# Optimization experiments

Measured on AMD Instinct MI355X. Metric: run time of the kernel, lower is better.

Reference implementation:

```python
import jax, jax.numpy as jnp
import numpy as np

EMBED = 1024
HEADS = 16
HEAD_DIM = EMBED // HEADS
MAX_SEQ = 5000
THETA = 10000.0
BATCH = 16
SEQ_K = 1024
SEQ_Q = 512


def _rope_tables():
    inv = 1.0 / (THETA ** (np.arange(0, EMBED, 2)[: EMBED // 2] / EMBED))
    ang = np.outer(np.arange(MAX_SEQ), inv)  # [MAX_SEQ, EMBED//2]
    return jnp.asarray(np.cos(ang), jnp.float32), jnp.asarray(np.sin(ang), jnp.float32)

COS_T, SIN_T = _rope_tables()


def _apply_rope(x, idx):
    # x: [B, S, E]; idx: [B, S]; pairs are (x[...,2i], x[...,2i+1]) across the FULL embed dim
    B, S, E = x.shape
    xp = x.reshape(B, S, E // 2, 2)
    xr, xi = xp[..., 0], xp[..., 1]
    c, s = COS_T[idx], SIN_T[idx]  # [B, S, E//2]
    return jnp.stack([xr * c - xi * s, xr * s + xi * c], axis=-1).reshape(B, S, E)


def _attn_mask(key_padding_mask):
    # (causal triu OR key padding) AND NOT eye  (eye keeps diagonal attendable), then cut query rows
    tri = jnp.triu(jnp.ones((SEQ_K, SEQ_K), bool), k=1)
    m = jnp.logical_or(tri[None], key_padding_mask[:, None, :])  # [B, K, K]
    m = jnp.logical_and(m, ~jnp.eye(SEQ_K, dtype=bool)[None])
    return m[:, -SEQ_Q:, :]  # [B, Q, K]


def setup_inputs() -> dict:
    key = jax.random.key(0)
    ks = jax.random.split(key, 16)
    def lin(i):
        W = jax.random.normal(ks[i], (EMBED, EMBED), jnp.float32) / np.sqrt(EMBED).astype(np.float32)
        b = jnp.zeros((EMBED,), jnp.float32)
        return W, b
    Wq, bq = lin(0); Wk, bk = lin(1); Wv, bv = lin(2); Wo, bo = lin(3)
    Wxr, bxr = lin(4); Wyr, byr = lin(5)
    Wxz, bxz = lin(6); Wyz, byz = lin(7)
    Wxg, bxg = lin(8); Wyg, byg = lin(9)
    key_in = jax.random.normal(ks[10], (BATCH, SEQ_K, EMBED), jnp.float32)
    key_index = jnp.sort(jax.random.randint(ks[11], (BATCH, SEQ_K), 0, MAX_SEQ), axis=-1)
    key_padding_mask = jax.random.randint(ks[12], (BATCH, SEQ_K), 0, 2).astype(bool)
    return dict(key_in=key_in, key_index=key_index, key_padding_mask=key_padding_mask,
                Wq=Wq, bq=bq, Wk=Wk, bk=bk, Wv=Wv, bv=bv, Wo=Wo, bo=bo,
                Wxr=Wxr, bxr=bxr, Wyr=Wyr, byr=byr, Wxz=Wxz, bxz=bxz,
                Wyz=Wyz, byz=byz, Wxg=Wxg, bxg=bxg, Wyg=Wyg, byg=byg)


def reference(key_in, key_index, key_padding_mask,
              Wq, bq, Wk, bk, Wv, bv, Wo, bo,
              Wxr, bxr, Wyr, byr, Wxz, bxz, Wyz, byz, Wxg, bxg, Wyg, byg):
    B = key_in.shape[0]
    # cut_query=True: query is the last SEQ_Q steps of key
    query = key_in[:, -SEQ_Q:]
    q_idx = key_index[:, -SEQ_Q:]
    q = query @ Wq + bq
    k = key_in @ Wk + bk
    v = key_in @ Wv + bv
    # RoPE applied on full embed dim BEFORE head split (as in source)
    q = _apply_rope(q, q_idx)
    k = _apply_rope(k, key_index)
    qh = q.reshape(B, SEQ_Q, HEADS, HEAD_DIM)
    kh = k.reshape(B, SEQ_K, HEADS, HEAD_DIM)
    vh = v.reshape(B, SEQ_K, HEADS, HEAD_DIM)
    mask = _attn_mask(key_padding_mask)  # [B, Q, K]
    bias = jnp.where(mask, -jnp.inf, 0.0).astype(key_in.dtype)[:, None]  # [B,1,Q,K]
    scores = jnp.einsum('bqhd,bkhd->bhqk', qh, kh) / np.float32(np.sqrt(HEAD_DIM)) + bias
    w = jax.nn.softmax(scores, axis=-1)  # [B,H,Q,K]
    o = jnp.einsum('bhqk,bkhd->bqhd', w, vh).reshape(B, SEQ_Q, EMBED)
    o = o @ Wo + bo
    # GRU-style gated residual combine (use_residual=True, use_gated=True)
    x = query
    r = jax.nn.sigmoid(x @ Wxr + bxr + o @ Wyr + byr)
    z = jax.nn.sigmoid(x @ Wxz + bxz + o @ Wyz + byz)
    h = jnp.tanh((r * x) @ Wxg + bxg + o @ Wyg + byg)
    out = (1.0 - z) * x + z * h
    attn_weights = w.mean(axis=1)  # averaged over heads, [B, Q, K]
    return out, attn_weights
```

## Files before the change

### kernel.cpp

```cpp
#include <hip/hip_runtime.h>
#include <hip/hip_bf16.h>


typedef __attribute__((ext_vector_type(8))) short bf16x8;
typedef __attribute__((ext_vector_type(4))) float f32x4;

__device__ __forceinline__ short f2bs(float f) {
  union { __hip_bfloat16 h; short s; } u; u.h = __float2bfloat16(f); return u.s;
}

static constexpr size_t OFF_WT   = 0;
static constexpr size_t OFF_TAB  = 20971520;
static constexpr size_t OFF_XBF  = 41451520;
static constexpr size_t OFF_QH   = 75005952;
static constexpr size_t OFF_KH   = 91783168;
static constexpr size_t OFF_VT   = 125337600;
static constexpr size_t OFF_OAT  = 158892032;
static constexpr size_t OFF_O2   = 175669248;
static constexpr size_t OFF_INV  = OFF_OAT;
static constexpr size_t OFF_RBZB = 75005952;
static constexpr size_t OFF_RX   = 142114816;
static constexpr size_t OFF_HB   = OFF_XBF;

__device__ __forceinline__ int swz(int q) { return ((q & 3) << 3) ^ ((q & 12) << 2); }

__global__ __launch_bounds__(256) void k_cvtx(const float* __restrict__ x,
                                              short* __restrict__ xbf) {
  size_t i = ((size_t)blockIdx.x * 256 + threadIdx.x) * 8;
  f32x4 a = *(const f32x4*)(x + i);
  f32x4 b = *(const f32x4*)(x + i + 4);
  bf16x8 o;
  o[0] = f2bs(a[0]); o[1] = f2bs(a[1]); o[2] = f2bs(a[2]); o[3] = f2bs(a[3]);
  o[4] = f2bs(b[0]); o[5] = f2bs(b[1]); o[6] = f2bs(b[2]); o[7] = f2bs(b[3]);
  *(bf16x8*)(xbf + i) = o;
}

__global__ void k_tabinv(double* __restrict__ inv) {
  int i = threadIdx.x;
  inv[i] = pow(10000.0, -(double)i / 512.0);
}
__global__ __launch_bounds__(256) void k_table(float* __restrict__ tab,
                                               const double* __restrict__ inv) {
  int i = blockIdx.x * 256 + threadIdx.x;
  if (i >= 5000 * 512) return;
  int pos = i >> 9, fi = i & 511;
  double ds, dc;
  sincos((double)pos * inv[fi], &ds, &dc);
  tab[2 * i] = (float)dc;
  tab[2 * i + 1] = (float)ds;
}

struct W10 { const float* p[10]; };
__global__ __launch_bounds__(256) void k_wt(W10 wsrc, short* __restrict__ wt) {
  __shared__ short t[32][33];
  int kb = blockIdx.x * 32, nb = blockIdx.y * 32, wi = blockIdx.z;
  const float* src = wsrc.p[wi];
  int tid = threadIdx.x;
#pragma unroll
  for (int e = 0; e < 4; ++e) {
    int idx = e * 256 + tid;
    int kr = idx >> 5, nc = idx & 31;
    t[nc][kr] = f2bs(src[(size_t)(kb + kr) * 1024 + nb + nc]);
  }
  __syncthreads();
  short* dst = wt + (size_t)wi * 1024 * 1024;
#pragma unroll
  for (int e = 0; e < 4; ++e) {
    int idx = e * 256 + tid;
    int nr = idx >> 5, kc = idx & 31;
    dst[(size_t)(nb + nr) * 1024 + kb + kc] = t[nr][kc];
  }
}

enum { CM_BF16 = 0, CM_F32 = 2, CM_F32ACC = 3, CM_VT = 4, CM_ROPE = 5 };

template <int AMODE, int CMODE>
__global__ __launch_bounds__(256) void k_gemm(
    const short* __restrict__ A, const short* __restrict__ Bt,
    const float* __restrict__ bias, const float* __restrict__ bias2,
    void* __restrict__ Cout, int ldc,
    const float* __restrict__ tab, const int* __restrict__ kidx,
    int sshift, int qoff) {
  __shared__ __align__(16) short lA[128 * 32];
  __shared__ __align__(16) short lB[128 * 32];
  const int tid = threadIdx.x;
  const int lane = tid & 63;
  const int wv = tid >> 6;
  const int wm = wv >> 1, wn = wv & 1;
  const int lo = lane & 15, hi = lane >> 4;
  const int tm0 = blockIdx.x * 128;
  const int tn0 = blockIdx.y * 128;

  const f32x4 vz = {0.f, 0.f, 0.f, 0.f};
  f32x4 acc[4][4];
#pragma unroll
  for (int m = 0; m < 4; ++m)
#pragma unroll
    for (int n = 0; n < 4; ++n) acc[m][n] = vz;

  for (int kt = 0; kt < 32; ++kt) {
    const int k0 = kt * 32;
    __syncthreads();
#pragma unroll
    for (int i = 0; i < 2; ++i) {
      int f = i * 256 + tid;
      int r = f >> 2;
      int cb = (f & 3) * 16;
      int arow = tm0 + r;
      if (AMODE) arow = ((arow >> 9) << 10) + 512 + (arow & 511);
      const char* ga = (const char*)(A + (size_t)arow * 1024 + k0) + cb;
      __builtin_amdgcn_global_load_lds(
          (const __attribute__((address_space(1))) void*)ga,
          (__attribute__((address_space(3))) void*)((char*)lA + (size_t)(i * 256 + wv * 64) * 16),
          16, 0, 0);
      int brow = tn0 + r;
      const char* gb = (const char*)(Bt + (size_t)brow * 1024 + k0) + cb;
      __builtin_amdgcn_global_load_lds(
          (const __attribute__((address_space(1))) void*)gb,
          (__attribute__((address_space(3))) void*)((char*)lB + (size_t)(i * 256 + wv * 64) * 16),
          16, 0, 0);
    }
    __syncthreads();
    bf16x8 af[4], bfr[4];
#pragma unroll
    for (int m = 0; m < 4; ++m)
      af[m] = *(const bf16x8*)&lA[(wm * 64 + m * 16 + lo) * 32 + hi * 8];
#pragma unroll
    for (int n = 0; n < 4; ++n)
      bfr[n] = *(const bf16x8*)&lB[(wn * 64 + n * 16 + lo) * 32 + hi * 8];
#pragma unroll
    for (int m = 0; m < 4; ++m)
#pragma unroll
      for (int n = 0; n < 4; ++n)
        acc[m][n] = __builtin_amdgcn_mfma_f32_16x16x32_bf16(af[m], bfr[n], acc[m][n], 0, 0, 0);
  }

  if constexpr (CMODE == CM_ROPE) {
    __hip_bfloat16* out = (__hip_bfloat16*)Cout;
    const float2* t2 = (const float2*)tab;
    const int srows = 1 << sshift;
    const float sgn = (lane & 1) ? 1.f : -1.f;
#pragma unroll
    for (int m = 0; m < 4; ++m) {
      int row_base = tm0 + wm * 64 + m * 16 + hi * 4;
#pragma unroll
      for (int n = 0; n < 4; ++n) {
        int col = tn0 + wn * 64 + n * 16 + lo;
        float bsv = bias[col];
        int j = col >> 1, hh = col >> 6, dd = col & 63;
#pragma unroll
        for (int r = 0; r < 4; ++r) {
          int row = row_base + r;
          int bb = row >> sshift, ss = row & (srows - 1);
          int idx = kidx[bb * 1024 + qoff + ss];
          float2 cs = t2[(size_t)idx * 512 + j];
          float val = acc[m][n][r] + bsv;
          float part = __shfl_xor(val, 1);
          float rot = val * cs.x + sgn * part * cs.y;
          out[((size_t)(bb * 16 + hh) * srows + ss) * 64 + dd] = __float2bfloat16(rot);
        }
      }
    }
  } else if constexpr (CMODE == CM_VT) {
    __hip_bfloat16* out = (__hip_bfloat16*)Cout;
#pragma unroll
    for (int m = 0; m < 4; ++m) {
      int row_base = tm0 + wm * 64 + m * 16 + hi * 4;
#pragma unroll
      for (int n = 0; n < 4; ++n) {
        int col = tn0 + wn * 64 + n * 16 + lo;
        float bsv = bias[col];
        int hh = col >> 6, dd = col & 63;
#pragma unroll
        for (int r = 0; r < 4; ++r) {
          int row = row_base + r;
          int bb = row >> 10, ss = row & 1023;
          out[((size_t)(bb * 16 + hh) * 64 + dd) * 1024 + ss] =
              __float2bfloat16(acc[m][n][r] + bsv);
        }
      }
    }
  } else if constexpr (CMODE == CM_F32 || CMODE == CM_F32ACC) {
    float* out = (float*)Cout;
#pragma unroll
    for (int m = 0; m < 4; ++m) {
      int row_base = tm0 + wm * 64 + m * 16 + hi * 4;
#pragma unroll
      for (int n = 0; n < 4; ++n) {
        int col = tn0 + wn * 64 + n * 16 + lo;
        float bsv = (col < 1024 || !bias2) ? bias[col] : bias2[col - 1024];
#pragma unroll
        for (int r = 0; r < 4; ++r) {
          size_t off = (size_t)(row_base + r) * ldc + col;
          float val = acc[m][n][r] + bsv;
          if constexpr (CMODE == CM_F32ACC) val += out[off];
          out[off] = val;
        }
      }
    }
  } else {
    __hip_bfloat16* out = (__hip_bfloat16*)Cout;
#pragma unroll
    for (int m = 0; m < 4; ++m) {
      int row_base = tm0 + wm * 64 + m * 16 + hi * 4;
#pragma unroll
      for (int n = 0; n < 4; ++n) {
        int col = tn0 + wn * 64 + n * 16 + lo;
        float bsv = bias[col];
#pragma unroll
        for (int r = 0; r < 4; ++r) {
          size_t off = (size_t)(row_base + r) * ldc + col;
          out[off] = __float2bfloat16(acc[m][n][r] + bsv);
        }
      }
    }
  }
}

__global__ __launch_bounds__(512, 2) void k_attn(
    const __hip_bfloat16* __restrict__ qh,
    const __hip_bfloat16* __restrict__ kh,
    const __hip_bfloat16* __restrict__ vt,
    const unsigned char* __restrict__ padraw,
    float* __restrict__ mean_out,
    __hip_bfloat16* __restrict__ oat) {
  __shared__ float Sld[16 * 1024];
  __shared__ float osc[4 * 64 * 4];
  short* Pld = (short*)Sld;
  const int wgid = blockIdx.x;
  const int b = wgid & 15, qt = wgid >> 4;
  const int tid = threadIdx.x, lane = tid & 63, wv = tid >> 6;
  const int lo = lane & 15, hi = lane >> 4;
  const int wg = wv & 3, half = wv >> 2;
  const f32x4 vz = {0.f, 0.f, 0.f, 0.f};

  bool is_byte = false;
#pragma unroll
  for (int j = 1; j < 256; ++j)
    if ((j & 3) && padraw[j] == 1) is_byte = true;
  const int* ipad = (const int*)padraw;

  unsigned pmask = 0;
#pragma unroll
  for (int nt = 0; nt < 8; ++nt) {
    int kpos = wv * 128 + nt * 16 + lo;
    int pk = is_byte ? (int)padraw[b * 1024 + kpos]
                     : (ipad[b * 1024 + kpos] != 0 ? 1 : 0);
    pmask |= (unsigned)(pk != 0) << nt;
  }

  float macc[2][16];
#pragma unroll
  for (int rr = 0; rr < 2; ++rr)
#pragma unroll
    for (int i = 0; i < 16; ++i) macc[rr][i] = 0.f;

  const __hip_bfloat16* qbase =
      qh + ((size_t)(b * 16) * 512 + (size_t)qt * 16) * 64;
  bf16x8 qf0 = *(const bf16x8*)(qbase + (size_t)lo * 64 + hi * 8);
  bf16x8 qf1 = *(const bf16x8*)(qbase + (size_t)lo * 64 + 32 + hi * 8);

  for (int h = 0; h < 16; ++h) {
    const __hip_bfloat16* kbh = kh + (size_t)(b * 16 + h) * 1024 * 64;
    const __hip_bfloat16* vbh = vt + (size_t)(b * 16 + h) * 64 * 1024;

    bf16x8 kbuf[2][2];
#pragma unroll
    for (int p = 0; p < 2; ++p) {
      int kr = wv * 128 + p * 16 + lo;
      kbuf[p][0] = *(const bf16x8*)(kbh + (size_t)kr * 64 + hi * 8);
      kbuf[p][1] = *(const bf16x8*)(kbh + (size_t)kr * 64 + 32 + hi * 8);
    }
#pragma unroll
    for (int nt = 0; nt < 8; ++nt) {
      bf16x8 ck0 = kbuf[nt & 1][0], ck1 = kbuf[nt & 1][1];
      if (nt < 6) {
        int kr = wv * 128 + (nt + 2) * 16 + lo;
        kbuf[nt & 1][0] = *(const bf16x8*)(kbh + (size_t)kr * 64 + hi * 8);
        kbuf[nt & 1][1] = *(const bf16x8*)(kbh + (size_t)kr * 64 + 32 + hi * 8);
      }
      f32x4 sa = vz;
      sa = __builtin_amdgcn_mfma_f32_16x16x32_bf16(qf0, ck0, sa, 0, 0, 0);
      sa = __builtin_amdgcn_mfma_f32_16x16x32_bf16(qf1, ck1, sa, 0, 0, 0);
      int kpos = wv * 128 + nt * 16 + lo;
      int pk = (pmask >> nt) & 1;
#pragma unroll
      for (int r = 0; r < 4; ++r) {
        int q = hi * 4 + r;
        int qg = 512 + qt * 16 + q;
        float sv = sa[r] * 0.125f;
        bool msk = (kpos > qg) || (kpos < qg && pk != 0);
        Sld[q * 1024 + (kpos ^ swz(q))] = msk ? -1e30f : sv;
      }
    }
    __syncthreads();

#pragma unroll
    for (int rr = 0; rr < 2; ++rr) {
      int q = wv * 2 + rr;
      const int c = swz(q);
      float* row = Sld + q * 1024;
      float v[16], mx = -1e30f;
#pragma unroll
      for (int i = 0; i < 16; ++i) {
        v[i] = row[(lane + i * 64) ^ c];
        mx = fmaxf(mx, v[i]);
      }
#pragma unroll
      for (int off = 32; off > 0; off >>= 1) mx = fmaxf(mx, __shfl_xor(mx, off));
      float sum = 0.f;
#pragma unroll
      for (int i = 0; i < 16; ++i) { v[i] = __expf(v[i] - mx); sum += v[i]; }
#pragma unroll
      for (int off = 32; off > 0; off >>= 1) sum += __shfl_xor(sum, off);
      float invs = 1.0f / sum;
      short* prow = Pld + q * 2048 + 1024;
#pragma unroll
      for (int i = 0; i < 16; ++i) {
        float p = v[i] * invs;
        prow[(lane + i * 64) ^ c] = f2bs(p);
        macc[rr][i] += p;
      }
    }
    __syncthreads();

    f32x4 oacc = vz;
    {
      const short* prow = Pld + lo * 2048 + 1024;
      const int cl = swz(lo);
      const int kcg = half * 16;
      const __hip_bfloat16* vrow = vbh + (size_t)(wg * 16 + lo) * 1024;
      bf16x8 vbuf[2];
#pragma unroll
      for (int p = 0; p < 2; ++p)
        vbuf[p] = *(const bf16x8*)(vrow + (kcg + p) * 32 + hi * 8);
#pragma unroll
      for (int kc = 0; kc < 16; ++kc) {
        bf16x8 cv = vbuf[kc & 1];
        if (kc < 14)
          vbuf[kc & 1] = *(const bf16x8*)(vrow + (kcg + kc + 2) * 32 + hi * 8);
        bf16x8 pa = *(const bf16x8*)&prow[((kcg + kc) * 32 + hi * 8) ^ cl];
        oacc = __builtin_amdgcn_mfma_f32_16x16x32_bf16(pa, cv, oacc, 0, 0, 0);
      }
    }

    if (h < 15) {
      const __hip_bfloat16* qn = qbase + (size_t)(h + 1) * 512 * 64;
      qf0 = *(const bf16x8*)(qn + (size_t)lo * 64 + hi * 8);
      qf1 = *(const bf16x8*)(qn + (size_t)lo * 64 + 32 + hi * 8);
    }

    if (half == 1) {
#pragma unroll
      for (int r = 0; r < 4; ++r) osc[(wg * 64 + lane) * 4 + r] = oacc[r];
    }
    __syncthreads();
    if (half == 0) {
#pragma unroll
      for (int r = 0; r < 4; ++r) {
        float o = oacc[r] + osc[(wg * 64 + lane) * 4 + r];
        int q = qt * 16 + hi * 4 + r;
        oat[((size_t)b * 512 + q) * 1024 + h * 64 + wg * 16 + lo] =
            __float2bfloat16(o);
      }
    }
  }

#pragma unroll
  for (int rr = 0; rr < 2; ++rr) {
    size_t mrow = ((size_t)b * 512 + (size_t)qt * 16 + wv * 2 + rr) * 1024;
#pragma unroll
    for (int i = 0; i < 16; ++i)
      mean_out[mrow + lane + i * 64] = macc[rr][i] * 0.0625f;
  }
}

__global__ __launch_bounds__(256) void k_rx(const float* __restrict__ RbZb,
                                            const float* __restrict__ x,
                                            short* __restrict__ rx) {
  size_t base = ((size_t)blockIdx.x * 256 + threadIdx.x) * 4;
  int row = (int)(base >> 10), col = (int)(base & 1023);
  int b = row >> 9, s = row & 511;
  const float* xp = x + ((size_t)(b * 1024 + 512 + s) << 10) + col;
  f32x4 rv = *(const f32x4*)(RbZb + (size_t)row * 2048 + col);
  f32x4 xv = *(const f32x4*)xp;
  typedef __attribute__((ext_vector_type(4))) short s16x4;
  s16x4 o;
#pragma unroll
  for (int j = 0; j < 4; ++j) {
    float r = 1.f / (1.f + __expf(-rv[j]));
    o[j] = f2bs(r * xv[j]);
  }
  *(s16x4*)(rx + base) = o;
}

__global__ __launch_bounds__(256) void k_final(const float* __restrict__ RbZb,
                                               const float* __restrict__ Hb,
                                               const float* __restrict__ x,
                                               float* __restrict__ out0) {
  size_t base = ((size_t)blockIdx.x * 256 + threadIdx.x) * 4;
  int row = (int)(base >> 10), col = (int)(base & 1023);
  int b = row >> 9, s = row & 511;
  const float* xp = x + ((size_t)(b * 1024 + 512 + s) << 10) + col;
  f32x4 zv = *(const f32x4*)(RbZb + (size_t)row * 2048 + 1024 + col);
  f32x4 hv = *(const f32x4*)(Hb + base);
  f32x4 xv = *(const f32x4*)xp;
  f32x4 o;
#pragma unroll
  for (int j = 0; j < 4; ++j) {
    float z = 1.f / (1.f + __expf(-zv[j]));
    float hh = tanhf(hv[j]);
    o[j] = (1.f - z) * xv[j] + z * hh;
  }
  *(f32x4*)(out0 + base) = o;
}

extern "C" void kernel_launch(void* const* d_in, const int* in_sizes, int n_in,
                              void* d_out, int out_size, void* d_ws, size_t ws_size,
                              hipStream_t stream) {
  const float* key_in = (const float*)d_in[0];
  const int* key_index = (const int*)d_in[1];
  const unsigned char* pad = (const unsigned char*)d_in[2];
  const float* bq  = (const float*)d_in[4];
  const float* bk  = (const float*)d_in[6];
  const float* bv  = (const float*)d_in[8];
  const float* bo  = (const float*)d_in[10];
  const float* bxr = (const float*)d_in[12];
  const float* byr = (const float*)d_in[14];
  const float* bxz = (const float*)d_in[16];
  const float* byz = (const float*)d_in[18];
  const float* bxg = (const float*)d_in[20];
  const float* byg = (const float*)d_in[22];

  char* ws = (char*)d_ws;
  short* wt = (short*)(ws + OFF_WT);
  float* tab = (float*)(ws + OFF_TAB);
  short* xbf = (short*)(ws + OFF_XBF);
  __hip_bfloat16* qh = (__hip_bfloat16*)(ws + OFF_QH);
  __hip_bfloat16* kh = (__hip_bfloat16*)(ws + OFF_KH);
  __hip_bfloat16* vt = (__hip_bfloat16*)(ws + OFF_VT);
  double* inv = (double*)(ws + OFF_INV);
  float* RbZb = (float*)(ws + OFF_RBZB);
  __hip_bfloat16* oat = (__hip_bfloat16*)(ws + OFF_OAT);
  short* o2 = (short*)(ws + OFF_O2);
  short* rx = (short*)(ws + OFF_RX);
  float* Hb = (float*)(ws + OFF_HB);

  float* out0 = (float*)d_out;
  float* out1 = out0 + (size_t)8388608;

  W10 wargs;
  wargs.p[0] = (const float*)d_in[3];
  wargs.p[1] = (const float*)d_in[5];
  wargs.p[2] = (const float*)d_in[7];
  wargs.p[3] = (const float*)d_in[9];
  wargs.p[4] = (const float*)d_in[11];
  wargs.p[5] = (const float*)d_in[15];
  wargs.p[6] = (const float*)d_in[13];
  wargs.p[7] = (const float*)d_in[17];
  wargs.p[8] = (const float*)d_in[19];
  wargs.p[9] = (const float*)d_in[21];

  k_cvtx<<<8192, 256, 0, stream>>>(key_in, xbf);
  k_wt<<<dim3(32, 32, 10), 256, 0, stream>>>(wargs, wt);
  k_tabinv<<<1, 512, 0, stream>>>(inv);
  k_table<<<10000, 256, 0, stream>>>(tab, inv);

  k_gemm<1, CM_ROPE><<<dim3(64, 8), 256, 0, stream>>>(
      xbf, wt + (size_t)0 * 1048576, bq, nullptr, (void*)qh, 0, tab, key_index, 9, 512);
  k_gemm<0, CM_ROPE><<<dim3(128, 8), 256, 0, stream>>>(
      xbf, wt + (size_t)1 * 1048576, bk, nullptr, (void*)kh, 0, tab, key_index, 10, 0);
  k_gemm<0, CM_VT><<<dim3(128, 8), 256, 0, stream>>>(
      xbf, wt + (size_t)2 * 1048576, bv, nullptr, (void*)vt, 0, nullptr, nullptr, 0, 0);

  k_attn<<<dim3(512), 512, 0, stream>>>(qh, kh, vt, pad, out1, oat);

  k_gemm<0, CM_BF16><<<dim3(64, 8), 256, 0, stream>>>(
      (const short*)oat, wt + (size_t)3 * 1048576, bo, nullptr, (void*)o2, 1024,
      nullptr, nullptr, 0, 0);
  k_gemm<1, CM_F32><<<dim3(64, 16), 256, 0, stream>>>(
      xbf, wt + (size_t)4 * 1048576, bxr, bxz, (void*)RbZb, 2048,
      nullptr, nullptr, 0, 0);
  k_gemm<0, CM_F32ACC><<<dim3(64, 16), 256, 0, stream>>>(
      o2, wt + (size_t)6 * 1048576, byr, byz, (void*)RbZb, 2048,
      nullptr, nullptr, 0, 0);
  k_rx<<<8192, 256, 0, stream>>>(RbZb, key_in, rx);
  k_gemm<0, CM_F32><<<dim3(64, 8), 256, 0, stream>>>(
      rx, wt + (size_t)8 * 1048576, bxg, nullptr, (void*)Hb, 1024,
      nullptr, nullptr, 0, 0);
  k_gemm<0, CM_F32ACC><<<dim3(64, 8), 256, 0, stream>>>(
      o2, wt + (size_t)9 * 1048576, byg, nullptr, (void*)Hb, 1024,
      nullptr, nullptr, 0, 0);
  k_final<<<8192, 256, 0, stream>>>(RbZb, Hb, key_in, out0);
}
```

Baseline: 768.4 us.

## Skip fully masked causal key tiles in attention QK, softmax and PV

After: 2.313 ms. 3.01x slower.

```diff
diff --git a/kernel.cpp b/kernel.cpp
--- a/kernel.cpp
+++ b/kernel.cpp
@@ -234,6 +234,11 @@
   const int wg = wv & 3, half = wv >> 2;
   const f32x4 vz = {0.f, 0.f, 0.f, 0.f};
 
+  const int gmax = 32 + qt;
+  const int nchunks = (gmax + 4) >> 2;
+  const int gpad = nchunks * 4 - 1;
+  const int ntv = ((gmax - wv) >> 3) + 1;
+
   bool is_byte = false;
 #pragma unroll
   for (int j = 1; j < 256; ++j)
@@ -243,7 +248,7 @@
   unsigned pmask = 0;
 #pragma unroll
   for (int nt = 0; nt < 8; ++nt) {
-    int kpos = wv * 128 + nt * 16 + lo;
+    int kpos = (nt * 8 + wv) * 16 + lo;
     int pk = is_byte ? (int)padraw[b * 1024 + kpos]
                      : (ipad[b * 1024 + kpos] != 0 ? 1 : 0);
     pmask |= (unsigned)(pk != 0) << nt;
@@ -264,25 +269,37 @@
     const __hip_bfloat16* kbh = kh + (size_t)(b * 16 + h) * 1024 * 64;
     const __hip_bfloat16* vbh = vt + (size_t)(b * 16 + h) * 64 * 1024;
 
+    for (int g = gmax + 1; g <= gpad; ++g) {
+      if ((g & 7) == wv) {
+        int kpos = g * 16 + lo;
+#pragma unroll
+        for (int r = 0; r < 4; ++r) {
+          int q = hi * 4 + r;
+          Sld[q * 1024 + (kpos ^ swz(q))] = -1e30f;
+        }
+      }
+    }
+
     bf16x8 kbuf[2][2];
 #pragma unroll
     for (int p = 0; p < 2; ++p) {
-      int kr = wv * 128 + p * 16 + lo;
+      int kr = (p * 8 + wv) * 16 + lo;
       kbuf[p][0] = *(const bf16x8*)(kbh + (size_t)kr * 64 + hi * 8);
       kbuf[p][1] = *(const bf16x8*)(kbh + (size_t)kr * 64 + 32 + hi * 8);
     }
 #pragma unroll
     for (int nt = 0; nt < 8; ++nt) {
+      if (nt >= ntv) break;
       bf16x8 ck0 = kbuf[nt & 1][0], ck1 = kbuf[nt & 1][1];
-      if (nt < 6) {
-        int kr = wv * 128 + (nt + 2) * 16 + lo;
+      if (nt + 2 < ntv) {
+        int kr = ((nt + 2) * 8 + wv) * 16 + lo;
         kbuf[nt & 1][0] = *(const bf16x8*)(kbh + (size_t)kr * 64 + hi * 8);
         kbuf[nt & 1][1] = *(const bf16x8*)(kbh + (size_t)kr * 64 + 32 + hi * 8);
       }
       f32x4 sa = vz;
       sa = __builtin_amdgcn_mfma_f32_16x16x32_bf16(qf0, ck0, sa, 0, 0, 0);
       sa = __builtin_amdgcn_mfma_f32_16x16x32_bf16(qf1, ck1, sa, 0, 0, 0);
-      int kpos = wv * 128 + nt * 16 + lo;
+      int kpos = (nt * 8 + wv) * 16 + lo;
       int pk = (pmask >> nt) & 1;
 #pragma unroll
       for (int r = 0; r < 4; ++r) {
@@ -303,6 +320,7 @@
       float v[16], mx = -1e30f;
 #pragma unroll
       for (int i = 0; i < 16; ++i) {
+        if (i >= nchunks) break;
         v[i] = row[(lane + i * 64) ^ c];
         mx = fmaxf(mx, v[i]);
       }
@@ -310,13 +328,18 @@
       for (int off = 32; off > 0; off >>= 1) mx = fmaxf(mx, __shfl_xor(mx, off));
       float sum = 0.f;
 #pragma unroll
-      for (int i = 0; i < 16; ++i) { v[i] = __expf(v[i] - mx); sum += v[i]; }
+      for (int i = 0; i < 16; ++i) {
+        if (i >= nchunks) break;
+        v[i] = __expf(v[i] - mx);
+        sum += v[i];
+      }
 #pragma unroll
       for (int off = 32; off > 0; off >>= 1) sum += __shfl_xor(sum, off);
       float invs = 1.0f / sum;
       short* prow = Pld + q * 2048 + 1024;
 #pragma unroll
       for (int i = 0; i < 16; ++i) {
+        if (i >= nchunks) break;
         float p = v[i] * invs;
         prow[(lane + i * 64) ^ c] = f2bs(p);
         macc[rr][i] += p;
@@ -328,18 +351,23 @@
     {
       const short* prow = Pld + lo * 2048 + 1024;
       const int cl = swz(lo);
-      const int kcg = half * 16;
       const __hip_bfloat16* vrow = vbh + (size_t)(wg * 16 + lo) * 1024;
       bf16x8 vbuf[2];
 #pragma unroll
-      for (int p = 0; p < 2; ++p)
-        vbuf[p] = *(const bf16x8*)(vrow + (kcg + p) * 32 + hi * 8);
-#pragma unroll
-      for (int kc = 0; kc < 16; ++kc) {
-        bf16x8 cv = vbuf[kc & 1];
-        if (kc < 14)
-          vbuf[kc & 1] = *(const bf16x8*)(vrow + (kcg + kc + 2) * 32 + hi * 8);
-        bf16x8 pa = *(const bf16x8*)&prow[((kcg + kc) * 32 + hi * 8) ^ cl];
+      for (int p = 0; p < 2; ++p) {
+        int kc = 2 * p + half;
+        vbuf[p] = *(const bf16x8*)(vrow + kc * 32 + hi * 8);
+      }
+#pragma unroll
+      for (int j = 0; j < 16; ++j) {
+        if (j >= nchunks) break;
+        int kc = 2 * j + half;
+        bf16x8 cv = vbuf[j & 1];
+        if (j + 2 < nchunks) {
+          int kcn = 2 * (j + 2) + half;
+          vbuf[j & 1] = *(const bf16x8*)(vrow + kcn * 32 + hi * 8);
+        }
+        bf16x8 pa = *(const bf16x8*)&prow[(kc * 32 + hi * 8) ^ cl];
         oacc = __builtin_amdgcn_mfma_f32_16x16x32_bf16(pa, cv, oacc, 0, 0, 0);
       }
     }
```
